# Kernel tuning notes

Hardware: AMD Instinct MI355X
Metric: run time of the kernel (lower is better)

The kernel has to match this reference:

```python
import jax, jax.numpy as jnp
import numpy as np

N, D_IN, D_OUT, E, K, H = 8192, 256, 256, 16, 2, 512


def setup_inputs() -> dict:
    key = jax.random.key(0)
    ks = jax.random.split(key, 11)
    return {
        "x": jax.random.normal(ks[0], (N, D_IN), jnp.float32),
        "gate_w": jax.random.normal(ks[1], (D_IN, H), jnp.float32),
        "gate_b": jax.random.normal(ks[2], (H,), jnp.float32),
        "gate_out_w": jax.random.normal(ks[3], (H, E), jnp.float32),
        "gate_out_b": jax.random.normal(ks[4], (E,), jnp.float32),
        "mlp_w1": jax.random.normal(ks[5], (D_IN, E, H), jnp.float32),
        "mlp_b1": jax.random.normal(ks[6], (E, H), jnp.float32),
        "mlp_w2": jax.random.normal(ks[7], (H, E, H), jnp.float32),
        "mlp_b2": jax.random.normal(ks[8], (E, H), jnp.float32),
        "mlp_w3": jax.random.normal(ks[9], (H, E, D_OUT), jnp.float32),
        "mlp_b3": jax.random.normal(ks[10], (E, D_OUT), jnp.float32),
    }


def reference(x, gate_w, gate_b, gate_out_w, gate_out_b,
              mlp_w1, mlp_b1, mlp_w2, mlp_b2, mlp_w3, mlp_b3):
    n, e = x.shape[0], gate_out_w.shape[1]
    # Gate MLP: relu(x @ Wg + bg) @ Wo + bo -> [N, E]
    logits = jax.nn.relu(x @ gate_w + gate_b) @ gate_out_w + gate_out_b
    # Top-k expert selection + softmax over selected gate values
    top_vals, top_idx = jax.lax.top_k(logits, K)              # [N, K]
    gates = jax.nn.softmax(top_vals, axis=-1)                 # [N, K]
    # Scatter into a sparse combine matrix [N, E] (top-k indices are unique per row)
    combine = jnp.zeros((n, e), x.dtype).at[jnp.arange(n)[:, None], top_idx].set(gates)
    # Per-expert 3-layer MLP, computed densely over all experts then combined.
    h1 = jax.nn.relu(jnp.einsum('ni,ieh->neh', x, mlp_w1) + mlp_b1)    # [N, E, H]
    h2 = jax.nn.relu(jnp.einsum('neh,heg->neg', h1, mlp_w2) + mlp_b2)  # [N, E, H]
    ye = jnp.einsum('neg,geo->neo', h2, mlp_w3) + mlp_b3               # [N, E, D_OUT]
    # Gate-weighted combine over experts (only top-k contribute)
    return jnp.einsum('neo,ne->no', ye, combine)
```

## Files before the change

kernel.cpp:

```cpp
#include <hip/hip_runtime.h>
#include <hip/hip_bf16.h>
#include <stdint.h>

#define NTOK 8192
#define DIN  256
#define DOUT 256
#define NEXP 16
#define HID  512
#define NKA  (NTOK*2)
#define NBLK (NTOK/256)
#define NRBLK (NTOK/8)
#define MAXTILE 272
#define GK 768

typedef __bf16 bf16x8 __attribute__((ext_vector_type(8)));
typedef __bf16 bf16x4 __attribute__((ext_vector_type(4)));
typedef float  f32x4  __attribute__((ext_vector_type(4)));

__device__ __forceinline__ void async_cp16(const __bf16* g, __bf16* l) {
  __builtin_amdgcn_global_load_lds(
      (const __attribute__((address_space(1))) unsigned int*)g,
      (__attribute__((address_space(3))) unsigned int*)l, 16, 0, 0);
}

__device__ __forceinline__ void transpose_cvt_body(const float* __restrict__ src,
                                                   __bf16* __restrict__ dst,
                                                   int K, int N, int bx, int by, int bz,
                                                   int tx, int ty, float (*t)[33]) {
  int e = bz, k0 = bx * 32, n0 = by * 32;
  #pragma unroll
  for (int j = 0; j < 4; j++) {
    int kl = ty + j * 8;
    t[kl][tx] = src[(size_t)(k0 + kl) * (NEXP * N) + (size_t)e * N + n0 + tx];
  }
  __syncthreads();
  #pragma unroll
  for (int j = 0; j < 4; j++) {
    int nl = ty + j * 8;
    dst[(size_t)e * N * K + (size_t)(n0 + nl) * K + k0 + tx] = (__bf16)t[tx][nl];
  }
}

__global__ __launch_bounds__(256) void prep_kernel(
    const float* __restrict__ x, __bf16* __restrict__ xb, __bf16* __restrict__ xs,
    const float* __restrict__ gw, __bf16* __restrict__ gwt,
    const float* __restrict__ w1, __bf16* __restrict__ w1t,
    const float* __restrict__ w2, __bf16* __restrict__ w2t,
    const float* __restrict__ w3, __bf16* __restrict__ w3t,
    int* __restrict__ gtile_e, int* __restrict__ gtile_mt,
    int* __restrict__ gntiles, int* __restrict__ gseg) {
  __shared__ float t[32][33];
  int idx = blockIdx.x;
  int tid = threadIdx.x;
  int tx = tid & 31, ty = tid >> 5;
  if (idx < 2048) {
    int i = idx * 256 + tid;
    float4 v = ((const float4*)x)[i];
    int base = i * 4;
    int tk = base >> 8, c = base & 255;
    bf16x4 hi = { (__bf16)v.x, (__bf16)v.y, (__bf16)v.z, (__bf16)v.w };
    bf16x4 lo = { (__bf16)(v.x - (float)hi[0]), (__bf16)(v.y - (float)hi[1]),
                  (__bf16)(v.z - (float)hi[2]), (__bf16)(v.w - (float)hi[3]) };
    *(bf16x4*)(xb + (size_t)tk * DIN + c) = hi;
    __bf16* row = xs + (size_t)tk * GK + c;
    *(bf16x4*)(row)       = hi;
    *(bf16x4*)(row + 256) = lo;
    *(bf16x4*)(row + 512) = hi;
  } else if (idx < 2176) {
    int g = idx - 2048;
    int k0 = (g & 7) * 32, n0 = (g >> 3) * 32;
    #pragma unroll
    for (int j = 0; j < 4; j++) {
      int kl = ty + j * 8;
      t[kl][tx] = gw[(size_t)(k0 + kl) * HID + n0 + tx];
    }
    __syncthreads();
    #pragma unroll
    for (int j = 0; j < 4; j++) {
      int nl = ty + j * 8;
      float v = t[tx][nl];
      __bf16 hi = (__bf16)v;
      __bf16 lo = (__bf16)(v - (float)hi);
      __bf16* drow = gwt + (size_t)(n0 + nl) * GK + k0 + tx;
      drow[0]   = hi;
      drow[256] = hi;
      drow[512] = lo;
    }
    if (g == 0) {
      if (tid < 128) { gtile_e[tid] = 0; gtile_mt[tid] = tid; }
      else if (tid == 128) { *gntiles = 128; }
      else if (tid == 129) { gseg[0] = 0; gseg[1] = NTOK; }
    }
  } else if (idx < 4224) {
    int g = idx - 2176;
    transpose_cvt_body(w1, w1t, DIN, HID, g & 7, (g >> 3) & 15, g >> 7, tx, ty, t);
  } else if (idx < 8320) {
    int g = idx - 4224;
    transpose_cvt_body(w2, w2t, HID, HID, g & 15, (g >> 4) & 15, g >> 8, tx, ty, t);
  } else {
    int g = idx - 8320;
    transpose_cvt_body(w3, w3t, HID, DOUT, g & 15, (g >> 4) & 7, g >> 7, tx, ty, t);
  }
}

__global__ __launch_bounds__(128) void route_kernel(const float* __restrict__ hg,
                                                    const float* __restrict__ gw,
                                                    const float* __restrict__ gb,
                                                    int2* __restrict__ e01,
                                                    float2* __restrict__ g01,
                                                    int* __restrict__ lrank,
                                                    int* __restrict__ blockhist) {
  __shared__ float hl[8][HID + 8];
  __shared__ float wl[HID][16];
  __shared__ float ls[8][16];
  __shared__ int bhist[NEXP];
  int t0 = blockIdx.x * 8;
  int tid = threadIdx.x;
  if (tid < NEXP) bhist[tid] = 0;
  for (int c = tid; c < 8 * (HID / 4); c += 128) {
    int row = c >> 7, col = (c & 127) * 4;
    *(float4*)&hl[row][col] = *(const float4*)&hg[(size_t)(t0 + row) * HID + col];
  }
  for (int c = tid; c < HID * 4; c += 128) {
    int k = c >> 2, e4 = (c & 3) * 4;
    *(float4*)&wl[k][e4] = *(const float4*)&gw[(size_t)k * 16 + e4];
  }
  __syncthreads();
  int tok = tid >> 4, e = tid & 15;
  float s = gb[e];
  #pragma unroll 8
  for (int k = 0; k < HID; k++) s = fmaf(hl[tok][k], wl[k][e], s);
  ls[tok][e] = s;
  __syncthreads();
  if (tid < 8) {
    int t = t0 + tid;
    float v0 = -3.402823466e38f, v1 = -3.402823466e38f;
    int i0 = 0, i1 = 0;
    #pragma unroll
    for (int ee = 0; ee < 16; ee++) {
      float v = ls[tid][ee];
      if (v > v0) { v1 = v0; i1 = i0; v0 = v; i0 = ee; }
      else if (v > v1) { v1 = v; i1 = ee; }
    }
    float ew = expf(v1 - v0);
    float inv = 1.f / (1.f + ew);
    e01[t] = make_int2(i0, i1);
    g01[t] = make_float2(inv, ew * inv);
    int r0 = atomicAdd(&bhist[i0], 1);
    int r1 = atomicAdd(&bhist[i1], 1);
    lrank[2 * t]     = r0;
    lrank[2 * t + 1] = r1;
  }
  __syncthreads();
  if (tid < NEXP) blockhist[blockIdx.x * NEXP + tid] = bhist[tid];
}

__global__ __launch_bounds__(256) void scan2_kernel(const int* __restrict__ blockhist,
                                                    int* __restrict__ offsets,
                                                    int* __restrict__ base,
                                                    int* __restrict__ tile_e,
                                                    int* __restrict__ tile_mt,
                                                    int* __restrict__ ntiles) {
  __shared__ int part[NEXP][16];
  __shared__ int cbase[NEXP][16];
  __shared__ int tot[NEXP];
  __shared__ int soff[NEXP + 1];
  __shared__ int tbase[NEXP];
  int tid = threadIdx.x;
  int e = tid & 15, c = tid >> 4;
  int s = 0;
  for (int i = 0; i < 64; i++) s += blockhist[(size_t)(c * 64 + i) * NEXP + e];
  part[e][c] = s;
  __syncthreads();
  if (tid < NEXP) {
    int t = 0;
    for (int c2 = 0; c2 < 16; c2++) { cbase[tid][c2] = t; t += part[tid][c2]; }
    tot[tid] = t;
  }
  __syncthreads();
  if (tid == 0) {
    int acc = 0, tb = 0;
    for (int i = 0; i < NEXP; i++) {
      soff[i] = acc; acc += tot[i];
      tbase[i] = tb; tb += (tot[i] + 63) >> 6;
    }
    soff[NEXP] = acc;
    *ntiles = tb;
  }
  __syncthreads();
  if (tid < NEXP + 1) offsets[tid] = soff[tid];
  {
    int run = soff[e] + cbase[e][c];
    for (int i = 0; i < 64; i++) {
      int b = c * 64 + i;
      base[(size_t)b * NEXP + e] = run;
      run += blockhist[(size_t)b * NEXP + e];
    }
  }
  if (tid < NEXP) {
    int nt = (tot[tid] + 63) >> 6, tb = tbase[tid];
    for (int m = 0; m < nt; m++) { tile_e[tb + m] = tid; tile_mt[tb + m] = m; }
  }
}

__global__ __launch_bounds__(256) void fill2_kernel(const int2* __restrict__ e01,
                                                    const int* __restrict__ lrank,
                                                    const int* __restrict__ base,
                                                    int* __restrict__ tok_sorted,
                                                    int* __restrict__ route_pos) {
  int t = blockIdx.x * 256 + threadIdx.x;
  int2 e = e01[t];
  int b = t >> 3;
  int p0 = base[(size_t)b * NEXP + e.x] + lrank[2 * t];
  int p1 = base[(size_t)b * NEXP + e.y] + lrank[2 * t + 1];
  tok_sorted[p0] = t; route_pos[2 * t]     = p0;
  tok_sorted[p1] = t; route_pos[2 * t + 1] = p1;
}

template<bool OUT_F32, bool RELU>
__global__ __launch_bounds__(256) void moe_gemm_kernel(const __bf16* __restrict__ A,
                                                       const __bf16* __restrict__ Bt,
                                                       const float* __restrict__ bias,
                                                       void* __restrict__ out,
                                                       const int* __restrict__ seg_off,
                                                       const int* __restrict__ gather,
                                                       const int* __restrict__ tile_e,
                                                       const int* __restrict__ tile_mt,
                                                       const int* __restrict__ ntiles,
                                                       int K, int N) {
  int bx = blockIdx.x;
  if (bx >= *ntiles) return;
  int e  = tile_e[bx];
  int mt = tile_mt[bx];
  int off = seg_off[e];
  int Te  = seg_off[e + 1] - off;
  int nt = blockIdx.y;

  __shared__ __bf16 Al[2][64][32];
  __shared__ __bf16 Bl[2][128][32];

  int tid = threadIdx.x;
  int lane = tid & 63, w = tid >> 6;
  int l16 = lane & 15, quad = lane >> 4;

  int r0 = tid >> 2;
  int q8 = ((tid & 3) ^ ((r0 >> 1) & 3)) * 8;
  int rowA = mt * 64 + r0;
  int rA = rowA < Te ? rowA : Te - 1;
  size_t ga = gather ? (size_t)gather[off + rA] : (size_t)(off + rA);
  const __bf16* apg  = A + ga * K + q8;
  const __bf16* Bte  = Bt + (size_t)e * N * K;
  const __bf16* bpg0 = Bte + (size_t)(nt * 128 + r0) * K + q8;
  const __bf16* bpg1 = bpg0 + (size_t)64 * K;

  __bf16* al0 = &Al[0][0][0];
  __bf16* al1 = &Al[1][0][0];
  __bf16* bl0 = &Bl[0][0][0];
  __bf16* bl1 = &Bl[1][0][0];

  f32x4 acc[4][2];
  #pragma unroll
  for (int i = 0; i < 4; i++)
    #pragma unroll
    for (int j = 0; j < 2; j++) acc[i][j] = {0.f, 0.f, 0.f, 0.f};

  async_cp16(apg, al0 + tid * 8);
  async_cp16(bpg0, bl0 + tid * 8);
  async_cp16(bpg1, bl0 + (tid + 256) * 8);

  int qs = (quad ^ ((l16 >> 1) & 3)) * 8;

  int nIter = K >> 5;
  for (int it = 0; it < nIter; ++it) {
    int buf = it & 1;
    if (it + 1 < nIter) {
      int kb = (it + 1) << 5;
      __bf16* an = buf ? al0 : al1;
      __bf16* bn = buf ? bl0 : bl1;
      async_cp16(apg + kb, an + tid * 8);
      async_cp16(bpg0 + kb, bn + tid * 8);
      async_cp16(bpg1 + kb, bn + (tid + 256) * 8);
      asm volatile("s_waitcnt vmcnt(3)" ::: "memory");
    } else {
      asm volatile("s_waitcnt vmcnt(0)" ::: "memory");
    }
    __builtin_amdgcn_s_barrier();
    asm volatile("" ::: "memory");
    const __bf16* ab = buf ? al1 : al0;
    const __bf16* bb = buf ? bl1 : bl0;
    bf16x8 af[4], bfr[2];
    #pragma unroll
    for (int i = 0; i < 4; i++)
      af[i] = *(const bf16x8*)(ab + (size_t)(i * 16 + l16) * 32 + qs);
    #pragma unroll
    for (int i = 0; i < 2; i++)
      bfr[i] = *(const bf16x8*)(bb + (size_t)(w * 32 + i * 16 + l16) * 32 + qs);
    #pragma unroll
    for (int mi = 0; mi < 4; mi++)
      #pragma unroll
      for (int ni = 0; ni < 2; ni++)
        acc[mi][ni] = __builtin_amdgcn_mfma_f32_16x16x32_bf16(af[mi], bfr[ni], acc[mi][ni], 0, 0, 0);
    asm volatile("" ::: "memory");
    __builtin_amdgcn_s_barrier();
  }

  const float* be = bias + (size_t)e * N;
  #pragma unroll
  for (int ni = 0; ni < 2; ni++) {
    int col = nt * 128 + w * 32 + ni * 16 + l16;
    float bv = be[col];
    #pragma unroll
    for (int mi = 0; mi < 4; mi++) {
      #pragma unroll
      for (int r = 0; r < 4; r++) {
        int row_in = mt * 64 + mi * 16 + quad * 4 + r;
        if (row_in < Te) {
          float v = acc[mi][ni][r] + bv;
          if (RELU) v = fmaxf(v, 0.f);
          size_t orow = (size_t)(off + row_in);
          if (OUT_F32) ((float*)out)[orow * N + col] = v;
          else ((__bf16*)out)[orow * N + col] = (__bf16)v;
        }
      }
    }
  }
}

__global__ void combine_kernel(const float* __restrict__ Y, const int* __restrict__ route_pos,
                               const float2* __restrict__ g01, float* __restrict__ out) {
  int gid = blockIdx.x * blockDim.x + threadIdx.x;
  int t = gid >> 6, c = (gid & 63) << 2;
  if (t >= NTOK) return;
  int p0 = route_pos[2 * t], p1 = route_pos[2 * t + 1];
  float2 g = g01[t];
  float4 y0 = *(const float4*)&Y[(size_t)p0 * DOUT + c];
  float4 y1 = *(const float4*)&Y[(size_t)p1 * DOUT + c];
  float4 o;
  o.x = g.x * y0.x + g.y * y1.x;
  o.y = g.x * y0.y + g.y * y1.y;
  o.z = g.x * y0.z + g.y * y1.z;
  o.w = g.x * y0.w + g.y * y1.w;
  *(float4*)&out[(size_t)t * DOUT + c] = o;
}

extern "C" void kernel_launch(void* const* d_in, const int* in_sizes, int n_in,
                              void* d_out, int out_size, void* d_ws, size_t ws_size,
                              hipStream_t stream) {
  const float* x          = (const float*)d_in[0];
  const float* gate_w     = (const float*)d_in[1];
  const float* gate_b     = (const float*)d_in[2];
  const float* gate_out_w = (const float*)d_in[3];
  const float* gate_out_b = (const float*)d_in[4];
  const float* w1         = (const float*)d_in[5];
  const float* b1         = (const float*)d_in[6];
  const float* w2         = (const float*)d_in[7];
  const float* b2         = (const float*)d_in[8];
  const float* w3         = (const float*)d_in[9];
  const float* b3         = (const float*)d_in[10];
  float* out = (float*)d_out;

  char* ws = (char*)d_ws;
  size_t o = 0;
  auto alloc = [&](size_t bytes) -> void* {
    o = (o + 255) & ~(size_t)255;
    void* p = ws + o;
    o += bytes;
    return p;
  };

  __bf16* xb   = (__bf16*)alloc((size_t)NTOK * DIN * 2);
  __bf16* w1t  = (__bf16*)alloc((size_t)NEXP * HID * DIN * 2);
  __bf16* w2t  = (__bf16*)alloc((size_t)NEXP * HID * HID * 2);
  __bf16* w3t  = (__bf16*)alloc((size_t)NEXP * DOUT * HID * 2);
  __bf16* gwt  = (__bf16*)alloc((size_t)HID * GK * 2);
  size_t r1 = (size_t)NTOK * HID * 4;
  size_t r2 = (size_t)(NKA + 128) * HID * 2;
  void* region1 = alloc(r1 > r2 ? r1 : r2);
  float*  hg = (float*)region1;
  __bf16* H1 = (__bf16*)region1;
  size_t r3 = (size_t)NTOK * GK * 2;
  size_t r4 = (size_t)(NKA + 128) * HID * 2;
  void* region2 = alloc(r3 > r4 ? r3 : r4);
  __bf16* xs = (__bf16*)region2;
  __bf16* H2 = (__bf16*)region2;
  int2*  e01       = (int2*)alloc((size_t)NTOK * 8);
  float2* g01      = (float2*)alloc((size_t)NTOK * 8);
  int*   offsets   = (int*)alloc((NEXP + 1) * 4);
  int*   blockhist = (int*)alloc((size_t)NRBLK * NEXP * 4);
  int*   base      = (int*)alloc((size_t)NRBLK * NEXP * 4);
  int*   lrank     = (int*)alloc((size_t)NTOK * 2 * 4);
  int*   tok_sorted= (int*)alloc((size_t)(NKA + 128) * 4);
  int*   route_pos = (int*)alloc((size_t)NTOK * 2 * 4);
  int*   tile_e    = (int*)alloc(MAXTILE * 4);
  int*   tile_mt   = (int*)alloc(MAXTILE * 4);
  int*   ntiles    = (int*)alloc(4);
  int*   gtile_e   = (int*)alloc(128 * 4);
  int*   gtile_mt  = (int*)alloc(128 * 4);
  int*   gntiles   = (int*)alloc(4);
  int*   gseg      = (int*)alloc(2 * 4);
  float*  Y        = (float*)alloc((size_t)(NKA + 128) * DOUT * 4);
  (void)ws_size; (void)n_in; (void)in_sizes; (void)out_size;

  prep_kernel<<<10368, 256, 0, stream>>>(x, xb, xs, gate_w, gwt,
                                         w1, w1t, w2, w2t, w3, w3t,
                                         gtile_e, gtile_mt, gntiles, gseg);

  moe_gemm_kernel<true, true><<<dim3(NTOK / 64, HID / 128), 256, 0, stream>>>(
      xs, gwt, gate_b, hg, gseg, nullptr, gtile_e, gtile_mt, gntiles, GK, HID);

  route_kernel<<<NTOK / 8, 128, 0, stream>>>(hg, gate_out_w, gate_out_b,
                                             e01, g01, lrank, blockhist);
  scan2_kernel<<<1, 256, 0, stream>>>(blockhist, offsets, base, tile_e, tile_mt, ntiles);
  fill2_kernel<<<NBLK, 256, 0, stream>>>(e01, lrank, base, tok_sorted, route_pos);

  moe_gemm_kernel<false, true><<<dim3(MAXTILE, HID / 128), 256, 0, stream>>>(
      xb, w1t, b1, H1, offsets, tok_sorted, tile_e, tile_mt, ntiles, DIN, HID);
  moe_gemm_kernel<false, true><<<dim3(MAXTILE, HID / 128), 256, 0, stream>>>(
      H1, w2t, b2, H2, offsets, nullptr, tile_e, tile_mt, ntiles, HID, HID);
  moe_gemm_kernel<true, false><<<dim3(MAXTILE, DOUT / 128), 256, 0, stream>>>(
      H2, w3t, b3, Y, offsets, nullptr, tile_e, tile_mt, ntiles, HID, DOUT);

  combine_kernel<<<(NTOK * 64) / 256, 256, 0, stream>>>(Y, route_pos, g01, out);
}
```

Measured before the change: 223.8 us.

## Fuse gated combine into last expert GEMM epilogue with atomic adds

Removes the separate combine kernel and the fp32 Y intermediate buffer. The third expert GEMM now scales each row by its gate weight and atomically adds it into the output at the original token row. The output is zeroed by extra blocks in the prep kernel, and gate weights are scattered into sorted order in fill2. This saves a kernel launch and the write and read of Y, but uses scalar float atomics, whose summation order is nondeterministic.

```diff
diff --git a/kernel.cpp b/kernel.cpp
--- a/kernel.cpp
+++ b/kernel.cpp
@@ -48,7 +48,8 @@
     const float* __restrict__ w2, __bf16* __restrict__ w2t,
     const float* __restrict__ w3, __bf16* __restrict__ w3t,
     int* __restrict__ gtile_e, int* __restrict__ gtile_mt,
-    int* __restrict__ gntiles, int* __restrict__ gseg) {
+    int* __restrict__ gntiles, int* __restrict__ gseg,
+    float* __restrict__ outz) {
   __shared__ float t[32][33];
   int idx = blockIdx.x;
   int tid = threadIdx.x;
@@ -97,9 +98,12 @@
   } else if (idx < 8320) {
     int g = idx - 4224;
     transpose_cvt_body(w2, w2t, HID, HID, g & 15, (g >> 4) & 15, g >> 8, tx, ty, t);
-  } else {
+  } else if (idx < 10368) {
     int g = idx - 8320;
     transpose_cvt_body(w3, w3t, HID, DOUT, g & 15, (g >> 4) & 7, g >> 7, tx, ty, t);
+  } else {
+    int i = (idx - 10368) * 256 + tid;
+    ((float4*)outz)[i] = make_float4(0.f, 0.f, 0.f, 0.f);
   }
 }
 
@@ -206,18 +210,21 @@
 __global__ __launch_bounds__(256) void fill2_kernel(const int2* __restrict__ e01,
                                                     const int* __restrict__ lrank,
                                                     const int* __restrict__ base,
+                                                    const float2* __restrict__ g01,
                                                     int* __restrict__ tok_sorted,
-                                                    int* __restrict__ route_pos) {
+                                                    int* __restrict__ route_pos,
+                                                    float* __restrict__ gw_sorted) {
   int t = blockIdx.x * 256 + threadIdx.x;
   int2 e = e01[t];
+  float2 g = g01[t];
   int b = t >> 3;
   int p0 = base[(size_t)b * NEXP + e.x] + lrank[2 * t];
   int p1 = base[(size_t)b * NEXP + e.y] + lrank[2 * t + 1];
-  tok_sorted[p0] = t; route_pos[2 * t]     = p0;
-  tok_sorted[p1] = t; route_pos[2 * t + 1] = p1;
-}
-
-template<bool OUT_F32, bool RELU>
+  tok_sorted[p0] = t; route_pos[2 * t]     = p0; gw_sorted[p0] = g.x;
+  tok_sorted[p1] = t; route_pos[2 * t + 1] = p1; gw_sorted[p1] = g.y;
+}
+
+template<int MODE, bool RELU>
 __global__ __launch_bounds__(256) void moe_gemm_kernel(const __bf16* __restrict__ A,
                                                        const __bf16* __restrict__ Bt,
                                                        const float* __restrict__ bias,
@@ -227,6 +234,8 @@
                                                        const int* __restrict__ tile_e,
                                                        const int* __restrict__ tile_mt,
                                                        const int* __restrict__ ntiles,
+                                                       const int* __restrict__ tok_s,
+                                                       const float* __restrict__ gws,
                                                        int K, int N) {
   int bx = blockIdx.x;
   if (bx >= *ntiles) return;
@@ -305,42 +314,48 @@
   }
 
   const float* be = bias + (size_t)e * N;
-  #pragma unroll
-  for (int ni = 0; ni < 2; ni++) {
-    int col = nt * 128 + w * 32 + ni * 16 + l16;
-    float bv = be[col];
+  if (MODE == 2) {
+    float bv[2];
+    #pragma unroll
+    for (int ni = 0; ni < 2; ni++) bv[ni] = be[nt * 128 + w * 32 + ni * 16 + l16];
     #pragma unroll
     for (int mi = 0; mi < 4; mi++) {
       #pragma unroll
       for (int r = 0; r < 4; r++) {
         int row_in = mt * 64 + mi * 16 + quad * 4 + r;
         if (row_in < Te) {
-          float v = acc[mi][ni][r] + bv;
-          if (RELU) v = fmaxf(v, 0.f);
-          size_t orow = (size_t)(off + row_in);
-          if (OUT_F32) ((float*)out)[orow * N + col] = v;
-          else ((__bf16*)out)[orow * N + col] = (__bf16)v;
+          int p = off + row_in;
+          int t = tok_s[p];
+          float gv = gws[p];
+          #pragma unroll
+          for (int ni = 0; ni < 2; ni++) {
+            int col = nt * 128 + w * 32 + ni * 16 + l16;
+            atomicAdd((float*)out + (size_t)t * N + col, (acc[mi][ni][r] + bv[ni]) * gv);
+          }
         }
       }
     }
-  }
-}
-
-__global__ void combine_kernel(const float* __restrict__ Y, const int* __restrict__ route_pos,
-                               const float2* __restrict__ g01, float* __restrict__ out) {
-  int gid = blockIdx.x * blockDim.x + threadIdx.x;
-  int t = gid >> 6, c = (gid & 63) << 2;
-  if (t >= NTOK) return;
-  int p0 = route_pos[2 * t], p1 = route_pos[2 * t + 1];
-  float2 g = g01[t];
-  float4 y0 = *(const float4*)&Y[(size_t)p0 * DOUT + c];
-  float4 y1 = *(const float4*)&Y[(size_t)p1 * DOUT + c];
-  float4 o;
-  o.x = g.x * y0.x + g.y * y1.x;
-  o.y = g.x * y0.y + g.y * y1.y;
-  o.z = g.x * y0.z + g.y * y1.z;
-  o.w = g.x * y0.w + g.y * y1.w;
-  *(float4*)&out[(size_t)t * DOUT + c] = o;
+  } else {
+    #pragma unroll
+    for (int ni = 0; ni < 2; ni++) {
+      int col = nt * 128 + w * 32 + ni * 16 + l16;
+      float bv = be[col];
+      #pragma unroll
+      for (int mi = 0; mi < 4; mi++) {
+        #pragma unroll
+        for (int r = 0; r < 4; r++) {
+          int row_in = mt * 64 + mi * 16 + quad * 4 + r;
+          if (row_in < Te) {
+            float v = acc[mi][ni][r] + bv;
+            if (RELU) v = fmaxf(v, 0.f);
+            size_t orow = (size_t)(off + row_in);
+            if (MODE == 1) ((float*)out)[orow * N + col] = v;
+            else ((__bf16*)out)[orow * N + col] = (__bf16)v;
+          }
+        }
+      }
+    }
+  }
 }
 
 extern "C" void kernel_launch(void* const* d_in, const int* in_sizes, int n_in,
@@ -391,6 +406,7 @@
   int*   lrank     = (int*)alloc((size_t)NTOK * 2 * 4);
   int*   tok_sorted= (int*)alloc((size_t)(NKA + 128) * 4);
   int*   route_pos = (int*)alloc((size_t)NTOK * 2 * 4);
+  float* gw_sorted = (float*)alloc((size_t)(NKA + 128) * 4);
   int*   tile_e    = (int*)alloc(MAXTILE * 4);
   int*   tile_mt   = (int*)alloc(MAXTILE * 4);
   int*   ntiles    = (int*)alloc(4);
@@ -398,27 +414,29 @@
   int*   gtile_mt  = (int*)alloc(128 * 4);
   int*   gntiles   = (int*)alloc(4);
   int*   gseg      = (int*)alloc(2 * 4);
-  float*  Y        = (float*)alloc((size_t)(NKA + 128) * DOUT * 4);
   (void)ws_size; (void)n_in; (void)in_sizes; (void)out_size;
 
-  prep_kernel<<<10368, 256, 0, stream>>>(x, xb, xs, gate_w, gwt,
+  prep_kernel<<<12416, 256, 0, stream>>>(x, xb, xs, gate_w, gwt,
                                          w1, w1t, w2, w2t, w3, w3t,
-                                         gtile_e, gtile_mt, gntiles, gseg);
-
-  moe_gemm_kernel<true, true><<<dim3(NTOK / 64, HID / 128), 256, 0, stream>>>(
-      xs, gwt, gate_b, hg, gseg, nullptr, gtile_e, gtile_mt, gntiles, GK, HID);
+                                         gtile_e, gtile_mt, gntiles, gseg, out);
+
+  moe_gemm_kernel<1, true><<<dim3(NTOK / 64, HID / 128), 256, 0, stream>>>(
+      xs, gwt, gate_b, hg, gseg, nullptr, gtile_e, gtile_mt, gntiles,
+      nullptr, nullptr, GK, HID);
 
   route_kernel<<<NTOK / 8, 128, 0, stream>>>(hg, gate_out_w, gate_out_b,
                                              e01, g01, lrank, blockhist);
   scan2_kernel<<<1, 256, 0, stream>>>(blockhist, offsets, base, tile_e, tile_mt, ntiles);
-  fill2_kernel<<<NBLK, 256, 0, stream>>>(e01, lrank, base, tok_sorted, route_pos);
-
-  moe_gemm_kernel<false, true><<<dim3(MAXTILE, HID / 128), 256, 0, stream>>>(
-      xb, w1t, b1, H1, offsets, tok_sorted, tile_e, tile_mt, ntiles, DIN, HID);
-  moe_gemm_kernel<false, true><<<dim3(MAXTILE, HID / 128), 256, 0, stream>>>(
-      H1, w2t, b2, H2, offsets, nullptr, tile_e, tile_mt, ntiles, HID, HID);
-  moe_gemm_kernel<true, false><<<dim3(MAXTILE, DOUT / 128), 256, 0, stream>>>(
-      H2, w3t, b3, Y, offsets, nullptr, tile_e, tile_mt, ntiles, HID, DOUT);
-
-  combine_kernel<<<(NTOK * 64) / 256, 256, 0, stream>>>(Y, route_pos, g01, out);
-}
+  fill2_kernel<<<NBLK, 256, 0, stream>>>(e01, lrank, base, g01,
+                                         tok_sorted, route_pos, gw_sorted);
+
+  moe_gemm_kernel<0, true><<<dim3(MAXTILE, HID / 128), 256, 0, stream>>>(
+      xb, w1t, b1, H1, offsets, tok_sorted, tile_e, tile_mt, ntiles,
+      nullptr, nullptr, DIN, HID);
+  moe_gemm_kernel<0, true><<<dim3(MAXTILE, HID / 128), 256, 0, stream>>>(
+      H1, w2t, b2, H2, offsets, nullptr, tile_e, tile_mt, ntiles,
+      nullptr, nullptr, HID, HID);
+  moe_gemm_kernel<2, false><<<dim3(MAXTILE, DOUT / 128), 256, 0, stream>>>(
+      H2, w3t, b3, out, offsets, nullptr, tile_e, tile_mt, ntiles,
+      tok_sorted, gw_sorted, HID, DOUT);
+}
```

Result: slower. 235.0 us (+5.0%).
